# Kernel tuning notes

Hardware: AMD Instinct MI355X
Metric: run time of the kernel (lower is better)

Reference implementation:

```python
import jax, jax.numpy as jnp
from jax import lax
import numpy as np

B, H, W = 8, 256, 256
NH = 128          # num_hiddens
NRH = 32          # num_residual_hiddens
K = 1024          # num_embeddings
D = 128           # embedding_dim
CC = 0.25         # commitment_cost


def setup_inputs() -> dict:
    key = jax.random.key(0)
    ks = jax.random.split(key, 18)

    def w(k, shape):
        fan_in = int(np.prod(shape[1:]))
        return (jax.random.normal(k, shape, jnp.float32) / np.sqrt(fan_in)).astype(jnp.float32)

    inp = {
        "x": jax.random.normal(ks[0], (B, 3, H, W), jnp.float32),
        # encoder
        "enc_c1": w(ks[1], (NH // 2, 3, 4, 4)),        # conv4x4 s2
        "enc_c2": w(ks[2], (NH, NH // 2, 4, 4)),       # conv4x4 s2
        "enc_c3": w(ks[3], (NH, NH, 3, 3)),            # conv3x3
        "enc_r1a": w(ks[4], (NRH, NH, 3, 3)),
        "enc_r1b": w(ks[5], (NH, NRH, 1, 1)),
        "enc_r2a": w(ks[6], (NRH, NH, 3, 3)),
        "enc_r2b": w(ks[7], (NH, NRH, 1, 1)),
        "pre_vq_w": w(ks[8], (D, NH, 1, 1)),
        # codebook: uniform(-1/K, 1/K) as in original init
        "codebook": jax.random.uniform(ks[9], (K, D), jnp.float32, -1.0 / K, 1.0 / K),
        # decoder
        "dec_c1": w(ks[10], (NH, D, 3, 3)),
        "dec_r1a": w(ks[11], (NRH, NH, 3, 3)),
        "dec_r1b": w(ks[12], (NH, NRH, 1, 1)),
        "dec_r2a": w(ks[13], (NRH, NH, 3, 3)),
        "dec_r2b": w(ks[14], (NH, NRH, 1, 1)),
        # ConvTranspose2d weight, torch layout [Cin, Cout, 4, 4]
        "dec_dc": w(ks[15], (NH, NH // 2, 4, 4)),
        "dec_c3": w(ks[16], (3, NH // 2, 3, 3)),
    }
    return inp


def _conv(x, w, s, p):
    return lax.conv_general_dilated(x, w, (s, s), ((p, p), (p, p)),
                                    dimension_numbers=("NCHW", "OIHW", "NCHW"))


def _deconv4x4_s2_p1(x, w_t):
    # torch ConvTranspose2d(k=4, s=2, p=1): flip kernel, swap in/out, lhs-dilate
    w = jnp.transpose(w_t[:, :, ::-1, ::-1], (1, 0, 2, 3))  # [Cout, Cin, 4, 4]
    return lax.conv_general_dilated(x, w, (1, 1), ((2, 2), (2, 2)),
                                    lhs_dilation=(2, 2),
                                    dimension_numbers=("NCHW", "OIHW", "NCHW"))


def _res_stack(x, r1a, r1b, r2a, r2b):
    for a, b in ((r1a, r1b), (r2a, r2b)):
        h = _conv(jax.nn.relu(x), a, 1, 1)
        h = _conv(jax.nn.relu(h), b, 1, 0)
        x = x + h
    return jax.nn.relu(x)


def _resize1d_align(x, axis, out_size):
    n = x.shape[axis]
    pos = jnp.arange(out_size, dtype=jnp.float32) * ((n - 1) / (out_size - 1))
    lo = jnp.floor(pos).astype(jnp.int32)
    hi = jnp.minimum(lo + 1, n - 1)
    wt = (pos - lo.astype(jnp.float32)).astype(x.dtype)
    shape = [1] * x.ndim
    shape[axis] = out_size
    wt = wt.reshape(shape)
    return jnp.take(x, lo, axis=axis) * (1 - wt) + jnp.take(x, hi, axis=axis) * wt


def _upsample2x_bilinear_align(x):  # align_corners=True, separable
    x = _resize1d_align(x, 2, 2 * x.shape[2])
    return _resize1d_align(x, 3, 2 * x.shape[3])


def reference(x, enc_c1, enc_c2, enc_c3, enc_r1a, enc_r1b, enc_r2a, enc_r2b,
              pre_vq_w, codebook, dec_c1, dec_r1a, dec_r1b, dec_r2a, dec_r2b,
              dec_dc, dec_c3):
    # ---- encoder ----
    h = jax.nn.relu(_conv(x, enc_c1, 2, 1))
    h = jax.nn.relu(_conv(h, enc_c2, 2, 1))
    h = _conv(h, enc_c3, 1, 1)            # note: no relu here (matches source)
    h = _res_stack(h, enc_r1a, enc_r1b, enc_r2a, enc_r2b)
    z = _conv(h, pre_vq_w, 1, 0)          # [B, D, H/4, W/4]

    # ---- VQ (eval mode: no EMA update, q_latent_loss = 0) ----
    zp = jnp.transpose(z, (0, 2, 3, 1))               # [B, h, w, D]
    flat = zp.reshape(-1, D)                          # [N, D]
    dist = (jnp.sum(flat * flat, axis=1, keepdims=True)
            + jnp.sum(codebook * codebook, axis=1)
            - 2.0 * flat @ codebook.T)                # [N, K]
    idx = jnp.argmin(dist, axis=1)                    # [N]
    q = codebook[idx].reshape(zp.shape)               # gather lookup
    e_latent_loss = jnp.mean((lax.stop_gradient(q) - zp) ** 2)
    loss = CC * e_latent_loss
    q_st = zp + lax.stop_gradient(q - zp)             # straight-through
    counts = jnp.zeros((K,), jnp.float32).at[idx].add(1.0)
    avg_probs = counts / flat.shape[0]
    perplexity = jnp.exp(-jnp.sum(avg_probs * jnp.log(avg_probs + 1e-10)))
    quantized = jnp.transpose(q_st, (0, 3, 1, 2))     # [B, D, h, w]

    # ---- decoder ----
    d = _conv(quantized, dec_c1, 1, 1)
    d = _res_stack(d, dec_r1a, dec_r1b, dec_r2a, dec_r2b)
    d = jax.nn.relu(_deconv4x4_s2_p1(d, dec_dc))
    d = _upsample2x_bilinear_align(d)
    d = _conv(d, dec_c3, 1, 1)
    recon = 2.0 * jax.nn.sigmoid(d) - 1.0             # [B, 3, H, W]
    return loss, recon, perplexity
```

## Files before the change

kernel.cpp:

```cpp
#include <hip/hip_runtime.h>
#include <hip/hip_bf16.h>
#include <math.h>

#define CC_COST 0.25

typedef __attribute__((ext_vector_type(8))) short short8v;
typedef __attribute__((ext_vector_type(4))) float f32x4;
typedef __attribute__((ext_vector_type(16))) float f32x16;

__device__ __forceinline__ unsigned short f2bf(float f) {
    unsigned u = __float_as_uint(f);
    unsigned r = (u + 0x7FFFu + ((u >> 16) & 1u)) >> 16;
    return (unsigned short)r;
}
__device__ __forceinline__ float bf2f(unsigned short h) {
    return __uint_as_float(((unsigned)h) << 16);
}


struct WtJobs {
    const float* src[15];
    float* dst[15];
    int cout[15], cin[15], kk[15], kind[15];
    int blk0[16];
};

__global__ void wt_batch_k(WtJobs J)
{
    int blk = blockIdx.x;
    int j = 0;
    while (j < 14 && blk >= J.blk0[j + 1]) ++j;
    int i = (blk - J.blk0[j]) * 256 + threadIdx.x;
    int total = J.cout[j] * J.cin[j] * J.kk[j];
    if (i >= total) return;
    const float* src = J.src[j];
    float* dst = J.dst[j];
    int kind = J.kind[j];
    if (kind == 0) {
        int Cout = J.cout[j], Cin = J.cin[j], KK = J.kk[j];
        int oc = i % Cout; int t2 = i / Cout; int t = t2 % KK; int c = t2 / KK;
        dst[i] = src[(oc * Cin + c) * KK + t];
    } else {
        int o = i % 3; int t = (i / 3) % 9; int c = i / 27;
        dst[i] = src[(o * 64 + c) * 9 + t];
    }
}

__global__ void wt_split_k(const float* __restrict__ w,
                           unsigned short* __restrict__ whi,
                           unsigned short* __restrict__ wlo)
{
    int i = blockIdx.x * 256 + threadIdx.x;
    if (i >= 147456) return;
    int ci = i & 15;
    int oc = (i >> 4) & 127;
    int rest = i >> 11;
    int cb = rest & 7;
    int tap = rest >> 3;
    float v = w[(oc * 128 + cb * 16 + ci) * 9 + tap];
    unsigned short h = f2bf(v);
    whi[i] = h;
    wlo[i] = f2bf(v - bf2f(h));
}

__global__ void wt_split4_k(const float* __restrict__ w,
                            unsigned short* __restrict__ whi,
                            unsigned short* __restrict__ wlo)
{
    int i = blockIdx.x * 256 + threadIdx.x;
    if (i >= 131072) return;
    int t = i & 15;
    int oc = (i >> 4) & 127;
    int rest = i >> 11;
    int cb = rest & 3;
    int tap = rest >> 2;
    float v = w[(oc * 64 + cb * 16 + t) * 16 + tap];
    unsigned short h = f2bf(v);
    whi[i] = h;
    wlo[i] = f2bf(v - bf2f(h));
}

__global__ void wt_split_dc_k(const float* __restrict__ w,
                              unsigned short* __restrict__ whi,
                              unsigned short* __restrict__ wlo)
{
    int i = blockIdx.x * 256 + threadIdx.x;
    if (i >= 131072) return;
    int ci = i & 15;
    int oc = (i >> 4) & 63;
    int cb = (i >> 10) & 7;
    int kx = (i >> 13) & 3;
    int ky = i >> 15;
    float v = w[((size_t)(cb * 16 + ci) * 64 + oc) * 16 + ky * 4 + kx];
    unsigned short h = f2bf(v);
    whi[i] = h;
    wlo[i] = f2bf(v - bf2f(h));
}

__global__ void wt_split_r_k(const float* __restrict__ w,
                             unsigned short* __restrict__ whi,
                             unsigned short* __restrict__ wlo)
{
    int i = blockIdx.x * 256 + threadIdx.x;
    if (i >= 36864) return;
    int k5 = i & 31;
    int oc = (i >> 5) & 31;
    int cb = (i >> 10) & 3;
    int tap = i >> 12;
    float v = w[(oc * 128 + cb * 32 + k5) * 9 + tap];
    unsigned short h = f2bf(v);
    whi[i] = h;
    wlo[i] = f2bf(v - bf2f(h));
}

__global__ __launch_bounds__(512) void conv3x3_mfma(
    const float* __restrict__ in,
    const unsigned short* __restrict__ whi,
    const unsigned short* __restrict__ wlo,
    float* __restrict__ out)
{
    constexpr int CST = 40;
    __shared__ unsigned short ls_hi[4 * 68 * CST];
    __shared__ unsigned short ls_lo[4 * 68 * CST];

    int tid = threadIdx.x;
    int lane = tid & 63;
    int w = tid >> 6;
    int myrow = w & 1;
    int oc0 = (w >> 1) * 32;
    int y0 = (blockIdx.x & 31) * 2;
    int b  = blockIdx.x >> 5;
    int ln31 = lane & 31;
    int lhf  = lane >> 5;

    f32x16 acc0 = {};
    f32x16 acc1 = {};

    const float* inb = in + (size_t)b * 128 * 4096;

    for (int chunk = 0; chunk < 4; ++chunk) {
        int c0 = chunk * 32;
        __syncthreads();
        for (int i = tid; i < 4 * 66 * 16; i += 512) {
            int x = i % 66;
            int t = i / 66;
            int cp = t & 15;
            int r = t >> 4;
            int gy = y0 - 1 + r, gx = x - 1;
            float v0 = 0.f, v1 = 0.f;
            if ((unsigned)gy < 64u && (unsigned)gx < 64u) {
                const float* p = inb + (size_t)(c0 + 2 * cp) * 4096 + gy * 64 + gx;
                v0 = p[0];
                v1 = p[4096];
            }
            unsigned short h0 = f2bf(v0), h1 = f2bf(v1);
            unsigned short l0 = f2bf(v0 - bf2f(h0)), l1 = f2bf(v1 - bf2f(h1));
            int a = (r * 68 + x) * CST + 2 * cp;
            *reinterpret_cast<unsigned int*>(&ls_hi[a]) = (unsigned)h0 | ((unsigned)h1 << 16);
            *reinterpret_cast<unsigned int*>(&ls_lo[a]) = (unsigned)l0 | ((unsigned)l1 << 16);
        }
        __syncthreads();

        #pragma unroll
        for (int tap = 0; tap < 9; ++tap) {
            int dy = tap / 3, dx = tap - 3 * (tap / 3);
            int rbase = (myrow + dy) * 68;
            #pragma unroll
            for (int cb = 0; cb < 2; ++cb) {
                int cbg = chunk * 2 + cb;
                size_t wofs = (((size_t)tap * 8 + cbg) * 128 + oc0 + ln31) * 16 + lhf * 8;
                short8v ah = *reinterpret_cast<const short8v*>(whi + wofs);
                short8v al = *reinterpret_cast<const short8v*>(wlo + wofs);
                int k0 = cb * 16 + lhf * 8;
                int xo0 = (rbase + ln31 + dx) * CST + k0;
                int xo1 = (rbase + 32 + ln31 + dx) * CST + k0;
                short8v bh0 = *reinterpret_cast<const short8v*>(&ls_hi[xo0]);
                short8v bl0 = *reinterpret_cast<const short8v*>(&ls_lo[xo0]);
                short8v bh1 = *reinterpret_cast<const short8v*>(&ls_hi[xo1]);
                short8v bl1 = *reinterpret_cast<const short8v*>(&ls_lo[xo1]);
                acc0 = __builtin_amdgcn_mfma_f32_32x32x16_bf16(ah, bh0, acc0, 0, 0, 0);
                acc1 = __builtin_amdgcn_mfma_f32_32x32x16_bf16(ah, bh1, acc1, 0, 0, 0);
                acc0 = __builtin_amdgcn_mfma_f32_32x32x16_bf16(ah, bl0, acc0, 0, 0, 0);
                acc1 = __builtin_amdgcn_mfma_f32_32x32x16_bf16(ah, bl1, acc1, 0, 0, 0);
                acc0 = __builtin_amdgcn_mfma_f32_32x32x16_bf16(al, bh0, acc0, 0, 0, 0);
                acc1 = __builtin_amdgcn_mfma_f32_32x32x16_bf16(al, bh1, acc1, 0, 0, 0);
            }
        }
    }

    float* ob = out + (size_t)b * 128 * 4096 + (size_t)(y0 + myrow) * 64;
    #pragma unroll
    for (int r = 0; r < 16; ++r) {
        int oc = oc0 + (r & 3) + 8 * (r >> 2) + 4 * lhf;
        ob[(size_t)oc * 4096 + ln31]      = acc0[r];
        ob[(size_t)oc * 4096 + 32 + ln31] = acc1[r];
    }
}

__global__ __launch_bounds__(512) void conv4x4s2_mfma(
    const float* __restrict__ in,
    const unsigned short* __restrict__ whi,
    const unsigned short* __restrict__ wlo,
    float* __restrict__ out)
{
    constexpr int CST = 24;
    __shared__ unsigned short lsEh[6 * 65 * CST];
    __shared__ unsigned short lsEl[6 * 65 * CST];
    __shared__ unsigned short lsOh[6 * 65 * CST];
    __shared__ unsigned short lsOl[6 * 65 * CST];

    int tid = threadIdx.x;
    int lane = tid & 63;
    int w = tid >> 6;
    int myrow = w & 1;
    int oc0 = (w >> 1) * 32;
    int y0 = (blockIdx.x & 31) * 2;
    int b  = blockIdx.x >> 5;
    int ln31 = lane & 31;
    int lhf  = lane >> 5;

    f32x16 acc0 = {};
    f32x16 acc1 = {};

    const float* inb = in + (size_t)b * 64 * 16384;

    for (int cb = 0; cb < 4; ++cb) {
        int c0 = cb * 16;
        __syncthreads();
        for (int i = tid; i < 12480; i += 512) {
            int gxi = i % 130; int t2 = i / 130;
            int r = t2 % 6; int cc = t2 / 6;
            int gx = gxi - 1;
            int gy = 2 * y0 - 1 + r;
            float v = 0.f;
            if ((unsigned)gy < 128u && (unsigned)gx < 128u)
                v = inb[(size_t)(c0 + cc) * 16384 + gy * 128 + gx];
            unsigned short h = f2bf(v);
            unsigned short l = f2bf(v - bf2f(h));
            if (gx & 1) {
                int a = (r * 65 + ((gx + 1) >> 1)) * CST + cc;
                lsOh[a] = h; lsOl[a] = l;
            } else {
                int a = (r * 65 + (gx >> 1)) * CST + cc;
                lsEh[a] = h; lsEl[a] = l;
            }
        }
        __syncthreads();

        #pragma unroll
        for (int tap = 0; tap < 16; ++tap) {
            int ky = tap >> 2, kx = tap & 3;
            int ridx = 2 * myrow + ky;
            int dlt = kx >> 1;
            const unsigned short* ph = (kx & 1) ? lsEh : lsOh;
            const unsigned short* pl = (kx & 1) ? lsEl : lsOl;
            size_t aoff = ((size_t)((tap * 4 + cb) * 128 + oc0 + ln31)) * 16 + lhf * 8;
            short8v ah = *reinterpret_cast<const short8v*>(whi + aoff);
            short8v al = *reinterpret_cast<const short8v*>(wlo + aoff);
            int base0 = (ridx * 65 + ln31 + dlt) * CST + lhf * 8;
            int base1 = (ridx * 65 + 32 + ln31 + dlt) * CST + lhf * 8;
            short8v bh0 = *reinterpret_cast<const short8v*>(ph + base0);
            short8v bl0 = *reinterpret_cast<const short8v*>(pl + base0);
            short8v bh1 = *reinterpret_cast<const short8v*>(ph + base1);
            short8v bl1 = *reinterpret_cast<const short8v*>(pl + base1);
            acc0 = __builtin_amdgcn_mfma_f32_32x32x16_bf16(ah, bh0, acc0, 0, 0, 0);
            acc1 = __builtin_amdgcn_mfma_f32_32x32x16_bf16(ah, bh1, acc1, 0, 0, 0);
            acc0 = __builtin_amdgcn_mfma_f32_32x32x16_bf16(ah, bl0, acc0, 0, 0, 0);
            acc1 = __builtin_amdgcn_mfma_f32_32x32x16_bf16(ah, bl1, acc1, 0, 0, 0);
            acc0 = __builtin_amdgcn_mfma_f32_32x32x16_bf16(al, bh0, acc0, 0, 0, 0);
            acc1 = __builtin_amdgcn_mfma_f32_32x32x16_bf16(al, bh1, acc1, 0, 0, 0);
        }
    }

    int y = y0 + myrow;
    float* ob = out + (size_t)b * 128 * 4096 + (size_t)y * 64;
    #pragma unroll
    for (int r = 0; r < 16; ++r) {
        int oc = oc0 + (r & 3) + 8 * (r >> 2) + 4 * lhf;
        ob[(size_t)oc * 4096 + ln31]      = fmaxf(acc0[r], 0.f);
        ob[(size_t)oc * 4096 + 32 + ln31] = fmaxf(acc1[r], 0.f);
    }
}

__global__ __launch_bounds__(512) void deconv_mfma(
    const float* __restrict__ in,
    const unsigned short* __restrict__ whi,
    const unsigned short* __restrict__ wlo,
    float* __restrict__ out)
{
    constexpr int CST = 40;
    __shared__ unsigned short ls_hi[3 * 68 * CST];
    __shared__ unsigned short ls_lo[3 * 68 * CST];

    int tid = threadIdx.x;
    int lane = tid & 63;
    int w = tid >> 6;
    int myrow = w & 1;
    int oc0 = ((w >> 1) & 1) * 32;
    int oxp = w >> 2;
    int yb = blockIdx.x & 63;
    int b  = blockIdx.x >> 6;
    int ln31 = lane & 31;
    int lhf  = lane >> 5;

    f32x16 acc0 = {};
    f32x16 acc1 = {};

    const float* inb = in + (size_t)b * 128 * 4096;

    for (int chunk = 0; chunk < 4; ++chunk) {
        int c0 = chunk * 32;
        __syncthreads();
        for (int i = tid; i < 3 * 66 * 16; i += 512) {
            int x = i % 66;
            int t = i / 66;
            int cp = t & 15;
            int r = t >> 4;
            int gy = yb - 1 + r, gx = x - 1;
            float v0 = 0.f, v1 = 0.f;
            if ((unsigned)gy < 64u && (unsigned)gx < 64u) {
                const float* p = inb + (size_t)(c0 + 2 * cp) * 4096 + gy * 64 + gx;
                v0 = fmaxf(p[0], 0.f);
                v1 = fmaxf(p[4096], 0.f);
            }
            unsigned short h0 = f2bf(v0), h1 = f2bf(v1);
            unsigned short l0 = f2bf(v0 - bf2f(h0)), l1 = f2bf(v1 - bf2f(h1));
            int a = (r * 68 + x) * CST + 2 * cp;
            *reinterpret_cast<unsigned int*>(&ls_hi[a]) = (unsigned)h0 | ((unsigned)h1 << 16);
            *reinterpret_cast<unsigned int*>(&ls_lo[a]) = (unsigned)l0 | ((unsigned)l1 << 16);
        }
        __syncthreads();

        #pragma unroll
        for (int tki = 0; tki < 2; ++tki) {
            int ky = (1 - myrow) + 2 * tki;
            int ldsrow = 1 + myrow - tki;
            #pragma unroll
            for (int txi = 0; txi < 2; ++txi) {
                int kx = (1 - oxp) + 2 * txi;
                int dlt = oxp - txi;
                #pragma unroll
                for (int cb = 0; cb < 2; ++cb) {
                    int cbg = chunk * 2 + cb;
                    size_t aoff = ((size_t)(((ky * 4 + kx) * 8 + cbg) * 64 + oc0 + ln31)) * 16 + lhf * 8;
                    short8v ah = *reinterpret_cast<const short8v*>(whi + aoff);
                    short8v al = *reinterpret_cast<const short8v*>(wlo + aoff);
                    int k0 = cb * 16 + lhf * 8;
                    int xo0 = (ldsrow * 68 + ln31 + dlt + 1) * CST + k0;
                    int xo1 = (ldsrow * 68 + 32 + ln31 + dlt + 1) * CST + k0;
                    short8v bh0 = *reinterpret_cast<const short8v*>(&ls_hi[xo0]);
                    short8v bl0 = *reinterpret_cast<const short8v*>(&ls_lo[xo0]);
                    short8v bh1 = *reinterpret_cast<const short8v*>(&ls_hi[xo1]);
                    short8v bl1 = *reinterpret_cast<const short8v*>(&ls_lo[xo1]);
                    acc0 = __builtin_amdgcn_mfma_f32_32x32x16_bf16(ah, bh0, acc0, 0, 0, 0);
                    acc1 = __builtin_amdgcn_mfma_f32_32x32x16_bf16(ah, bh1, acc1, 0, 0, 0);
                    acc0 = __builtin_amdgcn_mfma_f32_32x32x16_bf16(ah, bl0, acc0, 0, 0, 0);
                    acc1 = __builtin_amdgcn_mfma_f32_32x32x16_bf16(ah, bl1, acc1, 0, 0, 0);
                    acc0 = __builtin_amdgcn_mfma_f32_32x32x16_bf16(al, bh0, acc0, 0, 0, 0);
                    acc1 = __builtin_amdgcn_mfma_f32_32x32x16_bf16(al, bh1, acc1, 0, 0, 0);
                }
            }
        }
    }

    int oy = 2 * yb + myrow;
    float* ob = out + (size_t)b * 64 * 16384 + (size_t)oy * 128;
    #pragma unroll
    for (int r = 0; r < 16; ++r) {
        int oc = oc0 + (r & 3) + 8 * (r >> 2) + 4 * lhf;
        ob[(size_t)oc * 16384 + oxp + 2 * ln31]      = fmaxf(acc0[r], 0.f);
        ob[(size_t)oc * 16384 + oxp + 64 + 2 * ln31] = fmaxf(acc1[r], 0.f);
    }
}

__global__ __launch_bounds__(512) void conv3x3r_mfma(
    const float* __restrict__ in,
    const unsigned short* __restrict__ whi,
    const unsigned short* __restrict__ wlo,
    float* __restrict__ out)
{
    constexpr int CST = 40;
    __shared__ unsigned short ls_hi[3 * 68 * CST];
    __shared__ unsigned short ls_lo[3 * 68 * CST];

    int tid = threadIdx.x;
    int lane = tid & 63;
    int w = tid >> 6;
    int oc0 = (w & 1) * 16;
    int px0 = (w >> 1) * 16;
    int y = blockIdx.x & 63;
    int b = blockIdx.x >> 6;
    int n16 = lane & 15;
    int kk4 = lane >> 4;

    f32x4 acc = {};

    const float* inb = in + (size_t)b * 128 * 4096;

    for (int cb = 0; cb < 4; ++cb) {
        int c0 = cb * 32;
        __syncthreads();
        for (int i = tid; i < 3 * 66 * 16; i += 512) {
            int x = i % 66;
            int t = i / 66;
            int cp = t & 15;
            int r = t >> 4;
            int gy = y - 1 + r, gx = x - 1;
            float v0 = 0.f, v1 = 0.f;
            if ((unsigned)gy < 64u && (unsigned)gx < 64u) {
                const float* p = inb + (size_t)(c0 + 2 * cp) * 4096 + gy * 64 + gx;
                v0 = fmaxf(p[0], 0.f);
                v1 = fmaxf(p[4096], 0.f);
            }
            unsigned short h0 = f2bf(v0), h1 = f2bf(v1);
            unsigned short l0 = f2bf(v0 - bf2f(h0)), l1 = f2bf(v1 - bf2f(h1));
            int a = (r * 68 + x) * CST + 2 * cp;
            *reinterpret_cast<unsigned int*>(&ls_hi[a]) = (unsigned)h0 | ((unsigned)h1 << 16);
            *reinterpret_cast<unsigned int*>(&ls_lo[a]) = (unsigned)l0 | ((unsigned)l1 << 16);
        }
        __syncthreads();

        #pragma unroll
        for (int tap = 0; tap < 9; ++tap) {
            int dy = tap / 3, dx = tap - 3 * (tap / 3);
            size_t aoff = ((size_t)((tap * 4 + cb) * 32 + oc0 + n16)) * 32 + kk4 * 8;
            short8v ah = *reinterpret_cast<const short8v*>(whi + aoff);
            short8v al = *reinterpret_cast<const short8v*>(wlo + aoff);
            int xo = (dy * 68 + px0 + n16 + dx) * CST + kk4 * 8;
            short8v bh = *reinterpret_cast<const short8v*>(&ls_hi[xo]);
            short8v bl = *reinterpret_cast<const short8v*>(&ls_lo[xo]);
            acc = __builtin_amdgcn_mfma_f32_16x16x32_bf16(ah, bh, acc, 0, 0, 0);
            acc = __builtin_amdgcn_mfma_f32_16x16x32_bf16(ah, bl, acc, 0, 0, 0);
            acc = __builtin_amdgcn_mfma_f32_16x16x32_bf16(al, bh, acc, 0, 0, 0);
        }
    }

    float* ob = out + (size_t)b * 32 * 4096 + (size_t)y * 64;
    #pragma unroll
    for (int r = 0; r < 4; ++r) {
        int oc = oc0 + kk4 * 4 + r;
        ob[(size_t)oc * 4096 + px0 + n16] = acc[r];
    }
}

template<int CIN, int COUT, int CC, bool IN_RELU, bool ADD_RES>
__global__ __launch_bounds__(256) void conv1x1_k(
    const float* __restrict__ in, const float* __restrict__ wT,
    const float* __restrict__ res, float* __restrict__ out)
{
    static_assert(COUT == 128, "tile assumes 128");
    __shared__ __align__(16) float ls_in[CC][64];
    __shared__ __align__(16) float ls_w[CC][COUT];
    int tid = threadIdx.x;
    int pxg = tid & 7, ocg = tid >> 3;
    int x0 = pxg * 8, oc0 = ocg * 4;
    int y = blockIdx.x & 63, b = blockIdx.x >> 6;

    float acc[4][8];
    #pragma unroll
    for (int o = 0; o < 4; ++o)
        #pragma unroll
        for (int p = 0; p < 8; ++p) acc[o][p] = 0.f;

    for (int c0 = 0; c0 < CIN; c0 += CC) {
        __syncthreads();
        for (int i = tid; i < CC * 64; i += 256) {
            int xx = i & 63, cc = i >> 6;
            float v = in[(((size_t)b * CIN + c0 + cc) * 64 + y) * 64 + xx];
            if (IN_RELU) v = fmaxf(v, 0.f);
            ls_in[cc][xx] = v;
        }
        const float* wsrc = wT + (size_t)c0 * COUT;
        for (int i = tid; i < CC * COUT; i += 256)
            (&ls_w[0][0])[i] = wsrc[i];
        __syncthreads();

        for (int cc = 0; cc < CC; ++cc) {
            float rv[8];
            const float* base = &ls_in[cc][x0];
            float4 v0 = *reinterpret_cast<const float4*>(base);
            float4 v1 = *reinterpret_cast<const float4*>(base + 4);
            rv[0]=v0.x; rv[1]=v0.y; rv[2]=v0.z; rv[3]=v0.w;
            rv[4]=v1.x; rv[5]=v1.y; rv[6]=v1.z; rv[7]=v1.w;
            float4 w4 = *reinterpret_cast<const float4*>(&ls_w[cc][oc0]);
            float wv[4] = {w4.x, w4.y, w4.z, w4.w};
            #pragma unroll
            for (int p = 0; p < 8; ++p)
                #pragma unroll
                for (int o = 0; o < 4; ++o)
                    acc[o][p] = fmaf(rv[p], wv[o], acc[o][p]);
        }
    }
    #pragma unroll
    for (int o = 0; o < 4; ++o) {
        float* op = out + (((size_t)b * COUT + oc0 + o) * 64 + y) * 64 + x0;
        const float* rp = res + (((size_t)b * COUT + oc0 + o) * 64 + y) * 64 + x0;
        #pragma unroll
        for (int q = 0; q < 2; ++q) {
            float4 v = make_float4(acc[o][4*q], acc[o][4*q+1],
                                   acc[o][4*q+2], acc[o][4*q+3]);
            if (ADD_RES) {
                float4 r4 = *reinterpret_cast<const float4*>(rp + 4 * q);
                v.x += r4.x; v.y += r4.y; v.z += r4.z; v.w += r4.w;
            }
            *reinterpret_cast<float4*>(op + 4 * q) = v;
        }
    }
}

template<int CIN, int COUT, int WOUT, int CC, int OCB, int WOC, int NSLICE>
__global__ __launch_bounds__(256) void conv4x4s2_k(
    const float* __restrict__ in, const float* __restrict__ wT,
    float* __restrict__ out)
{
    constexpr int WIN = WOUT * 2;
    constexpr int NPXG = WOUT / 8, NOCG = COUT / OCB;
    static_assert(NPXG * NOCG == 256, "bad tile");
    constexpr int WUSE = 2 * WOUT + 2;
    constexpr int PADLEN = ((WUSE + (WUSE / 16 + 1) * 4) + 3) & ~3;
    __shared__ __align__(16) float ls_in[CC][4][PADLEN];
    __shared__ __align__(16) float ls_w[CC][16][COUT];

    int tid = threadIdx.x;
    int pxg = tid % NPXG, ocg = tid / NPXG;
    int x0 = pxg * 8, oc0 = ocg * OCB;
    int blk = blockIdx.x;
    int y = blk % WOUT; int rest = blk / WOUT;
    int slice = rest % NSLICE; int b = rest / NSLICE;
    int oc_base = slice * COUT;
    const float* inb = in + (size_t)b * CIN * WIN * WIN;

    float acc[OCB][8];
    #pragma unroll
    for (int o = 0; o < OCB; ++o)
        #pragma unroll
        for (int p = 0; p < 8; ++p) acc[o][p] = 0.f;

    for (int c0 = 0; c0 < CIN; c0 += CC) {
        __syncthreads();
        for (int i = tid; i < CC * 4 * WUSE; i += 256) {
            int xx = i % WUSE; int t = i / WUSE; int r = t & 3; int cc = t >> 2;
            int gy = 2 * y - 1 + r, gx = xx - 1;
            float v = 0.f;
            if ((unsigned)gy < (unsigned)WIN && (unsigned)gx < (unsigned)WIN)
                v = inb[(c0 + cc) * WIN * WIN + gy * WIN + gx];
            ls_in[cc][r][xx + ((xx >> 4) << 2)] = v;
        }
        const float* wsrc = wT + (size_t)c0 * 16 * WOC + oc_base;
        for (int i = tid; i < CC * 16 * COUT; i += 256) {
            int o = i % COUT; int tt = (i / COUT) % 16; int cc = i / (16 * COUT);
            ls_w[cc][tt][o] = wsrc[(cc * 16 + tt) * WOC + o];
        }
        __syncthreads();

        for (int cc = 0; cc < CC; ++cc) {
            const float* lw = &ls_w[cc][0][0];
            #pragma unroll
            for (int ky = 0; ky < 4; ++ky) {
                float rv[18];
                const float* base = &ls_in[cc][ky][20 * pxg];
                #pragma unroll
                for (int q = 0; q < 4; ++q) {
                    float4 v = *reinterpret_cast<const float4*>(base + 4 * q);
                    rv[4*q]=v.x; rv[4*q+1]=v.y; rv[4*q+2]=v.z; rv[4*q+3]=v.w;
                }
                rv[16] = base[20]; rv[17] = base[21];
                #pragma unroll
                for (int kx = 0; kx < 4; ++kx) {
                    const float* wp = lw + (ky * 4 + kx) * COUT + oc0;
                    float wv[OCB];
                    if constexpr (OCB == 4) {
                        float4 w4 = *reinterpret_cast<const float4*>(wp);
                        wv[0]=w4.x; wv[1]=w4.y; wv[2]=w4.z; wv[3]=w4.w;
                    } else {
                        float2 w2 = *reinterpret_cast<const float2*>(wp);
                        wv[0]=w2.x; wv[1]=w2.y;
                    }
                    #pragma unroll
                    for (int p = 0; p < 8; ++p) {
                        float iv = rv[2 * p + kx];
                        #pragma unroll
                        for (int o = 0; o < OCB; ++o)
                            acc[o][p] = fmaf(iv, wv[o], acc[o][p]);
                    }
                }
            }
        }
    }
    #pragma unroll
    for (int o = 0; o < OCB; ++o) {
        float* op = out + (((size_t)b * (COUT * NSLICE) + oc_base + oc0 + o) * WOUT + y) * WOUT + x0;
        #pragma unroll
        for (int q = 0; q < 2; ++q) {
            float4 v = make_float4(fmaxf(acc[o][4*q],0.f), fmaxf(acc[o][4*q+1],0.f),
                                   fmaxf(acc[o][4*q+2],0.f), fmaxf(acc[o][4*q+3],0.f));
            *reinterpret_cast<float4*>(op + 4 * q) = v;
        }
    }
}

template<int CC>
__global__ __launch_bounds__(256) void upconv_k(
    const float* __restrict__ in,
    const float* __restrict__ wT3,
    float* __restrict__ out)
{
    __shared__ __align__(16) float ls_u[CC][6][132];
    __shared__ float ls_w[64 * 27];
    __shared__ float xfx[132];
    __shared__ int   xloT[132];

    int tid = threadIdx.x;
    int row = tid >> 6;
    int pxl = tid & 63;
    int blk = blockIdx.x;
    int xh = blk & 1;
    int yblk = (blk >> 1) & 63;
    int b = blk >> 7;
    int xbase = xh * 128;
    int y0 = yblk * 4, y = y0 + row;
    const float SCL = 127.0f / 255.0f;
    const float* hb = in + (size_t)b * 64 * 16384;

    for (int i = tid; i < 1728; i += 256) ls_w[i] = wT3[i];
    if (tid < 130) {
        int ux = xbase - 1 + tid;
        bool v = ((unsigned)ux < 256u);
        float px = (v ? ux : 0) * SCL;
        int lo = (int)px;
        xloT[tid] = lo;
        xfx[tid] = v ? (px - (float)lo) : -1.0f;
    }

    float acc[3][2];
    #pragma unroll
    for (int o = 0; o < 3; ++o) { acc[o][0] = 0.f; acc[o][1] = 0.f; }

    for (int c0 = 0; c0 < 64; c0 += CC) {
        __syncthreads();
        for (int i = tid; i < CC * 6 * 130; i += 256) {
            int xx = i % 130; int t = i / 130; int r = t % 6; int cc = t / 6;
            int uy = y0 - 1 + r;
            float v = 0.f;
            float fx = xfx[xx];
            if ((unsigned)uy < 256u && fx >= 0.f) {
                float py = uy * SCL;
                int ylo = (int)py; int yhi = min(ylo + 1, 127); float fy = py - (float)ylo;
                int lo = xloT[xx]; int hi = min(lo + 1, 127);
                const float* hp = hb + (size_t)(c0 + cc) * 16384 + ylo * 128;
                const float* hq = hb + (size_t)(c0 + cc) * 16384 + yhi * 128;
                float a = hp[lo], b2 = hp[hi], c2 = hq[lo], d2 = hq[hi];
                float top = a + (b2 - a) * fx;
                float bot = c2 + (d2 - c2) * fx;
                v = top + (bot - top) * fy;
            }
            ls_u[cc][r][xx] = v;
        }
        __syncthreads();

        for (int cc = 0; cc < CC; ++cc) {
            #pragma unroll
            for (int j = 0; j < 3; ++j) {
                const float* base = &ls_u[cc][row + j][pxl * 2];
                float2 a0 = *reinterpret_cast<const float2*>(base);
                float2 a1 = *reinterpret_cast<const float2*>(base + 2);
                float rv[4] = {a0.x, a0.y, a1.x, a1.y};
                #pragma unroll
                for (int i2 = 0; i2 < 3; ++i2) {
                    const float* wp = &ls_w[((c0 + cc) * 9 + (j * 3 + i2)) * 3];
                    float w0 = wp[0], w1 = wp[1], w2 = wp[2];
                    #pragma unroll
                    for (int p = 0; p < 2; ++p) {
                        float iv = rv[p + i2];
                        acc[0][p] = fmaf(iv, w0, acc[0][p]);
                        acc[1][p] = fmaf(iv, w1, acc[1][p]);
                        acc[2][p] = fmaf(iv, w2, acc[2][p]);
                    }
                }
            }
        }
    }
    int x0 = xbase + pxl * 2;
    #pragma unroll
    for (int o = 0; o < 3; ++o) {
        float2 v;
        v.x = 2.f / (1.f + expf(-acc[o][0])) - 1.f;
        v.y = 2.f / (1.f + expf(-acc[o][1])) - 1.f;
        float* op = out + (((size_t)b * 3 + o) * 256 + y) * 256 + x0;
        *reinterpret_cast<float2*>(op) = v;
    }
}

__global__ void prep_codebook(const float* __restrict__ cb,
                              unsigned short* __restrict__ cbh,
                              unsigned short* __restrict__ cbl,
                              float* __restrict__ ce2,
                              unsigned int* __restrict__ counts)
{
    int k = blockIdx.x * 256 + threadIdx.x;
    if (k >= 1024) return;
    float s = 0.f;
    for (int d = 0; d < 128; ++d) {
        float v = cb[k * 128 + d];
        s = fmaf(v, v, s);
        unsigned short h = f2bf(v);
        int kk = d >> 4, t = d & 15;
        cbh[(kk * 1024 + k) * 16 + t] = h;
        cbl[(kk * 1024 + k) * 16 + t] = f2bf(v - bf2f(h));
    }
    ce2[k] = s;
    counts[k] = 0u;
}

__global__ __launch_bounds__(512) void vq_fused(
    const float* __restrict__ z, const float* __restrict__ cb,
    const unsigned short* __restrict__ cbh,
    const unsigned short* __restrict__ cbl,
    const float* __restrict__ ce2,
    unsigned int* __restrict__ counts, float* __restrict__ q,
    double* __restrict__ partial)
{
    constexpr int ZP = 136;
    __shared__ unsigned short zh[64 * ZP];
    __shared__ unsigned short zlo[64 * ZP];
    __shared__ float ce2l[1024];
    __shared__ float cmbd[4][2][32];
    __shared__ int   cmbi[4][2][32];
    __shared__ int sidx[64];
    __shared__ float red[8];

    int tid = threadIdx.x;
    int lane = tid & 63;
    int w = tid >> 6;
    int pxg = w & 1;
    int cgrp = w >> 1;
    int ln31 = lane & 31;
    int lhf = lane >> 5;
    int p0g = blockIdx.x * 64;
    int b = p0g >> 12;
    int p0 = p0g & 4095;

    for (int i = tid; i < 8192; i += 512) {
        int d = i >> 6, px = i & 63;
        float v = z[((size_t)b * 128 + d) * 4096 + p0 + px];
        unsigned short h = f2bf(v);
        zh[px * ZP + d]  = h;
        zlo[px * ZP + d] = f2bf(v - bf2f(h));
    }
    for (int i = tid; i < 1024; i += 512) ce2l[i] = ce2[i];
    __syncthreads();

    int pxrow = pxg * 32 + ln31;
    short8v zfh[8], zfl[8];
    #pragma unroll
    for (int kk = 0; kk < 8; ++kk) {
        int off = pxrow * ZP + kk * 16 + lhf * 8;
        zfh[kk] = *reinterpret_cast<const short8v*>(&zh[off]);
        zfl[kk] = *reinterpret_cast<const short8v*>(&zlo[off]);
    }

    float best = 3.4e38f; int bidx = 0;
    #pragma unroll
    for (int ct = 0; ct < 8; ++ct) {
        int c0 = cgrp * 256 + ct * 32;
        f32x16 acc = {};
        #pragma unroll
        for (int kk = 0; kk < 8; ++kk) {
            size_t aoff = ((size_t)(kk * 1024 + c0 + ln31)) * 16 + lhf * 8;
            short8v ah = *reinterpret_cast<const short8v*>(cbh + aoff);
            short8v al = *reinterpret_cast<const short8v*>(cbl + aoff);
            acc = __builtin_amdgcn_mfma_f32_32x32x16_bf16(ah, zfh[kk], acc, 0, 0, 0);
            acc = __builtin_amdgcn_mfma_f32_32x32x16_bf16(ah, zfl[kk], acc, 0, 0, 0);
            acc = __builtin_amdgcn_mfma_f32_32x32x16_bf16(al, zfh[kk], acc, 0, 0, 0);
        }
        #pragma unroll
        for (int r = 0; r < 16; ++r) {
            int code = c0 + (r & 3) + 8 * (r >> 2) + 4 * lhf;
            float dist = ce2l[code] - 2.f * acc[r];
            if (dist < best || (dist == best && code < bidx)) { best = dist; bidx = code; }
        }
    }
    {
        float ob = __shfl_xor(best, 32);
        int   oi = __shfl_xor(bidx, 32);
        if (ob < best || (ob == best && oi < bidx)) { best = ob; bidx = oi; }
    }
    if (lane < 32) { cmbd[cgrp][pxg][lane] = best; cmbi[cgrp][pxg][lane] = bidx; }
    __syncthreads();
    if (tid < 64) {
        int pg = tid >> 5, l = tid & 31;
        float bv = cmbd[0][pg][l]; int bi = cmbi[0][pg][l];
        #pragma unroll
        for (int g = 1; g < 4; ++g) {
            float ov = cmbd[g][pg][l]; int oi = cmbi[g][pg][l];
            if (ov < bv || (ov == bv && oi < bi)) { bv = ov; bi = oi; }
        }
        sidx[pg * 32 + l] = bi;
        atomicAdd(&counts[bi], 1u);
    }
    __syncthreads();

    int pix = tid & 63, dg = tid >> 6;
    int kidx = sidx[pix];
    const float* crow = cb + (size_t)kidx * 128 + dg * 16;
    float sq = 0.f;
    size_t zbase = ((size_t)b * 128 + dg * 16) * 4096 + p0 + pix;
    #pragma unroll
    for (int ii = 0; ii < 4; ++ii) {
        float4 c4 = *reinterpret_cast<const float4*>(crow + 4 * ii);
        float vals[4] = {c4.x, c4.y, c4.z, c4.w};
        #pragma unroll
        for (int jj = 0; jj < 4; ++jj) {
            int dl = ii * 4 + jj;
            float qv = vals[jj];
            float zv = z[zbase + (size_t)dl * 4096];
            float df = qv - zv;
            sq = fmaf(df, df, sq);
            q[zbase + (size_t)dl * 4096] = qv;
        }
    }
    #pragma unroll
    for (int off = 32; off > 0; off >>= 1) sq += __shfl_xor(sq, off);
    if (lane == 0) red[w] = sq;
    __syncthreads();
    if (tid == 0) {
        double s = 0.0;
        #pragma unroll
        for (int ww = 0; ww < 8; ++ww) s += (double)red[ww];
        partial[blockIdx.x] = s;
    }
}

__global__ __launch_bounds__(256) void finalize_kernel(
    const double* __restrict__ partial, const unsigned int* __restrict__ counts,
    float* __restrict__ dout)
{
    __shared__ double sd[256];
    __shared__ double lossSh;
    int tid = threadIdx.x;
    double s = 0.0;
    for (int i = tid; i < 512; i += 256) s += partial[i];
    sd[tid] = s; __syncthreads();
    for (int off = 128; off > 0; off >>= 1) {
        if (tid < off) sd[tid] += sd[tid + off];
        __syncthreads();
    }
    if (tid == 0) lossSh = CC_COST * sd[0] / 4194304.0;
    __syncthreads();

    double h = 0.0;
    for (int k = tid; k < 1024; k += 256) {
        double pp = (double)counts[k] / 32768.0;
        h += pp * log(pp + 1e-10);
    }
    sd[tid] = h; __syncthreads();
    for (int off = 128; off > 0; off >>= 1) {
        if (tid < off) sd[tid] += sd[tid + off];
        __syncthreads();
    }
    if (tid == 0) {
        dout[0]       = (float)lossSh;
        dout[1572865] = (float)exp(-sd[0]);
    }
}

extern "C" void kernel_launch(void* const* d_in, const int* in_sizes, int n_in,
                              void* d_out, int out_size, void* d_ws, size_t ws_size,
                              hipStream_t stream)
{
    const float* x        = (const float*)d_in[0];
    const float* enc_c1   = (const float*)d_in[1];
    const float* enc_c2   = (const float*)d_in[2];
    const float* enc_c3   = (const float*)d_in[3];
    const float* enc_r1a  = (const float*)d_in[4];
    const float* enc_r1b  = (const float*)d_in[5];
    const float* enc_r2a  = (const float*)d_in[6];
    const float* enc_r2b  = (const float*)d_in[7];
    const float* pre_vq_w = (const float*)d_in[8];
    const float* codebook = (const float*)d_in[9];
    const float* dec_c1   = (const float*)d_in[10];
    const float* dec_r1a  = (const float*)d_in[11];
    const float* dec_r1b  = (const float*)d_in[12];
    const float* dec_r2a  = (const float*)d_in[13];
    const float* dec_r2b  = (const float*)d_in[14];
    const float* dec_dc   = (const float*)d_in[15];
    const float* dec_c3   = (const float*)d_in[16];
    float* dout = (float*)d_out;

    char* wsp = (char*)d_ws;
    auto alloc = [&](size_t bytes) {
        void* p = (void*)wsp;
        wsp += (bytes + 255) & ~(size_t)255;
        return p;
    };
    float* h1   = (float*)alloc(8ull*64*128*128*4);
    float* bufA = (float*)alloc(8ull*128*64*64*4);
    float* bufB = (float*)alloc(8ull*128*64*64*4);
    float* bufT = (float*)alloc(8ull*32*64*64*4);
    unsigned short* cbh = (unsigned short*)alloc(131072*2);
    unsigned short* cbl = (unsigned short*)alloc(131072*2);
    float* ce2  = (float*)alloc(1024*4);
    unsigned int* counts = (unsigned int*)alloc(1024*4);
    double* partial = (double*)alloc(512*8);
    float* wt_ec1  = (float*)alloc(3072*4);
    float* wt_er1b = (float*)alloc(4096*4);
    float* wt_er2b = (float*)alloc(4096*4);
    float* wt_pvq  = (float*)alloc(16384*4);
    float* wt_dr1b = (float*)alloc(4096*4);
    float* wt_dr2b = (float*)alloc(4096*4);
    float* wt_dc3  = (float*)alloc(1728*4);
    unsigned short* w3hi_e = (unsigned short*)alloc(147456*2);
    unsigned short* w3lo_e = (unsigned short*)alloc(147456*2);
    unsigned short* w3hi_d = (unsigned short*)alloc(147456*2);
    unsigned short* w3lo_d = (unsigned short*)alloc(147456*2);
    unsigned short* w4hi   = (unsigned short*)alloc(131072*2);
    unsigned short* w4lo   = (unsigned short*)alloc(131072*2);
    unsigned short* wdchi  = (unsigned short*)alloc(131072*2);
    unsigned short* wdclo  = (unsigned short*)alloc(131072*2);
    unsigned short* wr1aeh = (unsigned short*)alloc(36864*2);
    unsigned short* wr1ael = (unsigned short*)alloc(36864*2);
    unsigned short* wr2aeh = (unsigned short*)alloc(36864*2);
    unsigned short* wr2ael = (unsigned short*)alloc(36864*2);
    unsigned short* wr1adh = (unsigned short*)alloc(36864*2);
    unsigned short* wr1adl = (unsigned short*)alloc(36864*2);
    unsigned short* wr2adh = (unsigned short*)alloc(36864*2);
    unsigned short* wr2adl = (unsigned short*)alloc(36864*2);
    float* zb = bufA;
    float* qb = h1;

    prep_codebook<<<4, 256, 0, stream>>>(codebook, cbh, cbl, ce2, counts);

    WtJobs J;
    const float* srcs[7] = {enc_c1, enc_r1b, enc_r2b, pre_vq_w,
                            dec_r1b, dec_r2b, dec_c3};
    float* dsts[7] = {wt_ec1, wt_er1b, wt_er2b, wt_pvq,
                      wt_dr1b, wt_dr2b, wt_dc3};
    int couts[7] = {64, 128, 128, 128, 128, 128, 3};
    int cins[7]  = {3, 32, 32, 128, 32, 32, 64};
    int kks[7]   = {16, 1, 1, 1, 1, 1, 9};
    int kinds[7] = {0, 0, 0, 0, 0, 0, 2};
    int off = 0;
    for (int j = 0; j < 7; ++j) {
        J.src[j] = srcs[j]; J.dst[j] = dsts[j];
        J.cout[j] = couts[j]; J.cin[j] = cins[j]; J.kk[j] = kks[j];
        J.kind[j] = kinds[j];
        J.blk0[j] = off;
        off += (couts[j] * cins[j] * kks[j] + 255) / 256;
    }
    J.blk0[7] = off;
    for (int j = 8; j < 16; ++j) J.blk0[j] = off + 1000000;
    wt_batch_k<<<off, 256, 0, stream>>>(J);
    wt_split_k<<<576, 256, 0, stream>>>(enc_c3, w3hi_e, w3lo_e);
    wt_split_k<<<576, 256, 0, stream>>>(dec_c1, w3hi_d, w3lo_d);
    wt_split4_k<<<512, 256, 0, stream>>>(enc_c2, w4hi, w4lo);
    wt_split_dc_k<<<512, 256, 0, stream>>>(dec_dc, wdchi, wdclo);
    wt_split_r_k<<<144, 256, 0, stream>>>(enc_r1a, wr1aeh, wr1ael);
    wt_split_r_k<<<144, 256, 0, stream>>>(enc_r2a, wr2aeh, wr2ael);
    wt_split_r_k<<<144, 256, 0, stream>>>(dec_r1a, wr1adh, wr1adl);
    wt_split_r_k<<<144, 256, 0, stream>>>(dec_r2a, wr2adh, wr2adl);

    conv4x4s2_k<3, 64, 128, 3, 4, 64, 1><<<1024, 256, 0, stream>>>(x, wt_ec1, h1);
    conv4x4s2_mfma<<<256, 512, 0, stream>>>(h1, w4hi, w4lo, bufA);
    conv3x3_mfma<<<256, 512, 0, stream>>>(bufA, w3hi_e, w3lo_e, bufB);
    conv3x3r_mfma<<<512, 512, 0, stream>>>(bufB, wr1aeh, wr1ael, bufT);
    conv1x1_k<32, 128, 32, true, true><<<512, 256, 0, stream>>>(bufT, wt_er1b, bufB, bufB);
    conv3x3r_mfma<<<512, 512, 0, stream>>>(bufB, wr2aeh, wr2ael, bufT);
    conv1x1_k<32, 128, 32, true, true><<<512, 256, 0, stream>>>(bufT, wt_er2b, bufB, bufB);
    conv1x1_k<128, 128, 32, true, false><<<512, 256, 0, stream>>>(bufB, wt_pvq, bufB, zb);

    vq_fused<<<512, 512, 0, stream>>>(zb, codebook, cbh, cbl, ce2, counts, qb, partial);

    conv3x3_mfma<<<256, 512, 0, stream>>>(qb, w3hi_d, w3lo_d, bufA);
    conv3x3r_mfma<<<512, 512, 0, stream>>>(bufA, wr1adh, wr1adl, bufT);
    conv1x1_k<32, 128, 32, true, true><<<512, 256, 0, stream>>>(bufT, wt_dr1b, bufA, bufA);
    conv3x3r_mfma<<<512, 512, 0, stream>>>(bufA, wr2adh, wr2adl, bufT);
    conv1x1_k<32, 128, 32, true, true><<<512, 256, 0, stream>>>(bufT, wt_dr2b, bufA, bufA);
    deconv_mfma<<<512, 512, 0, stream>>>(bufA, wdchi, wdclo, h1);
    upconv_k<8><<<1024, 256, 0, stream>>>(h1, wt_dc3, dout + 1);

    finalize_kernel<<<1, 256, 0, stream>>>(partial, counts, dout);
}
```

Baseline: 788.3 us.

## Fuse residual 3x3 and 1x1 convs into one MFMA kernel; retile upconv

Each residual block's 3x3 conv (128->32) and 1x1 conv (32->128) plus residual add now run in one kernel. The intermediate goes through LDS as split bf16 hi/lo and feeds a 32x32 MFMA with precomputed split 1x1 weights. This removes the bufT round trip and four kernel launches, and the result is written to a ping-pong buffer instead of in place. Separately, upconv now computes one pixel per thread over 2 rows with a smaller channel chunk and twice the blocks. That trades some register reuse for lower LDS use and more parallelism.

```diff
diff --git a/kernel.cpp b/kernel.cpp
--- a/kernel.cpp
+++ b/kernel.cpp
@@ -108,6 +108,21 @@
     int cb = (i >> 10) & 3;
     int tap = i >> 12;
     float v = w[(oc * 128 + cb * 32 + k5) * 9 + tap];
+    unsigned short h = f2bf(v);
+    whi[i] = h;
+    wlo[i] = f2bf(v - bf2f(h));
+}
+
+__global__ void wt_split_1x1_k(const float* __restrict__ w,
+                               unsigned short* __restrict__ whi,
+                               unsigned short* __restrict__ wlo)
+{
+    int i = blockIdx.x * 256 + threadIdx.x;
+    if (i >= 4096) return;
+    int ci = i & 15;
+    int oc = (i >> 4) & 127;
+    int kk = i >> 11;
+    float v = w[oc * 32 + kk * 16 + ci];
     unsigned short h = f2bf(v);
     whi[i] = h;
     wlo[i] = f2bf(v - bf2f(h));
@@ -373,10 +388,12 @@
     }
 }
 
-__global__ __launch_bounds__(512) void conv3x3r_mfma(
+__global__ __launch_bounds__(512) void fused_res_k(
     const float* __restrict__ in,
     const unsigned short* __restrict__ whi,
     const unsigned short* __restrict__ wlo,
+    const unsigned short* __restrict__ w1hi,
+    const unsigned short* __restrict__ w1lo,
     float* __restrict__ out)
 {
     constexpr int CST = 40;
@@ -392,9 +409,10 @@
     int b = blockIdx.x >> 6;
     int n16 = lane & 15;
     int kk4 = lane >> 4;
+    int ln31 = lane & 31;
+    int lhf = lane >> 5;
 
     f32x4 acc = {};
-
     const float* inb = in + (size_t)b * 128 * 4096;
 
     for (int cb = 0; cb < 4; ++cb) {
@@ -435,11 +453,41 @@
         }
     }
 
-    float* ob = out + (size_t)b * 32 * 4096 + (size_t)y * 64;
+    __syncthreads();
     #pragma unroll
     for (int r = 0; r < 4; ++r) {
-        int oc = oc0 + kk4 * 4 + r;
-        ob[(size_t)oc * 4096 + px0 + n16] = acc[r];
+        int ch = oc0 + kk4 * 4 + r;
+        int px = px0 + n16;
+        float v = fmaxf(acc[r], 0.f);
+        unsigned short h = f2bf(v);
+        ls_hi[px * CST + ch] = h;
+        ls_lo[px * CST + ch] = f2bf(v - bf2f(h));
+    }
+    __syncthreads();
+
+    int oc1 = (w & 3) * 32;
+    int pxt = (w >> 2) * 32;
+    f32x16 acc2 = {};
+    #pragma unroll
+    for (int kk = 0; kk < 2; ++kk) {
+        size_t aoff = ((size_t)(kk * 128 + oc1 + ln31)) * 16 + lhf * 8;
+        short8v ah = *reinterpret_cast<const short8v*>(w1hi + aoff);
+        short8v al = *reinterpret_cast<const short8v*>(w1lo + aoff);
+        int boff = (pxt + ln31) * CST + kk * 16 + lhf * 8;
+        short8v bh = *reinterpret_cast<const short8v*>(&ls_hi[boff]);
+        short8v bl = *reinterpret_cast<const short8v*>(&ls_lo[boff]);
+        acc2 = __builtin_amdgcn_mfma_f32_32x32x16_bf16(ah, bh, acc2, 0, 0, 0);
+        acc2 = __builtin_amdgcn_mfma_f32_32x32x16_bf16(ah, bl, acc2, 0, 0, 0);
+        acc2 = __builtin_amdgcn_mfma_f32_32x32x16_bf16(al, bh, acc2, 0, 0, 0);
+    }
+
+    float* ob = out + (size_t)b * 128 * 4096 + (size_t)y * 64;
+    const float* rb = inb + (size_t)y * 64;
+    #pragma unroll
+    for (int r = 0; r < 16; ++r) {
+        int oc = oc1 + (r & 3) + 8 * (r >> 2) + 4 * lhf;
+        size_t o = (size_t)oc * 4096 + pxt + ln31;
+        ob[o] = rb[o] + acc2[r];
     }
 }
 
@@ -605,20 +653,20 @@
     const float* __restrict__ wT3,
     float* __restrict__ out)
 {
-    __shared__ __align__(16) float ls_u[CC][6][132];
+    __shared__ __align__(16) float ls_u[CC][4][132];
     __shared__ float ls_w[64 * 27];
     __shared__ float xfx[132];
     __shared__ int   xloT[132];
 
     int tid = threadIdx.x;
-    int row = tid >> 6;
-    int pxl = tid & 63;
+    int row = tid >> 7;
+    int pxl = tid & 127;
     int blk = blockIdx.x;
     int xh = blk & 1;
-    int yblk = (blk >> 1) & 63;
-    int b = blk >> 7;
+    int yblk = (blk >> 1) & 127;
+    int b = blk >> 8;
     int xbase = xh * 128;
-    int y0 = yblk * 4, y = y0 + row;
+    int y0 = yblk * 2, y = y0 + row;
     const float SCL = 127.0f / 255.0f;
     const float* hb = in + (size_t)b * 64 * 16384;
 
@@ -632,14 +680,12 @@
         xfx[tid] = v ? (px - (float)lo) : -1.0f;
     }
 
-    float acc[3][2];
-    #pragma unroll
-    for (int o = 0; o < 3; ++o) { acc[o][0] = 0.f; acc[o][1] = 0.f; }
+    float acc[3] = {0.f, 0.f, 0.f};
 
     for (int c0 = 0; c0 < 64; c0 += CC) {
         __syncthreads();
-        for (int i = tid; i < CC * 6 * 130; i += 256) {
-            int xx = i % 130; int t = i / 130; int r = t % 6; int cc = t / 6;
+        for (int i = tid; i < CC * 4 * 130; i += 256) {
+            int xx = i % 130; int t = i / 130; int r = t & 3; int cc = t >> 2;
             int uy = y0 - 1 + r;
             float v = 0.f;
             float fx = xfx[xx];
@@ -661,33 +707,26 @@
         for (int cc = 0; cc < CC; ++cc) {
             #pragma unroll
             for (int j = 0; j < 3; ++j) {
-                const float* base = &ls_u[cc][row + j][pxl * 2];
-                float2 a0 = *reinterpret_cast<const float2*>(base);
-                float2 a1 = *reinterpret_cast<const float2*>(base + 2);
-                float rv[4] = {a0.x, a0.y, a1.x, a1.y};
-                #pragma unroll
-                for (int i2 = 0; i2 < 3; ++i2) {
-                    const float* wp = &ls_w[((c0 + cc) * 9 + (j * 3 + i2)) * 3];
-                    float w0 = wp[0], w1 = wp[1], w2 = wp[2];
-                    #pragma unroll
-                    for (int p = 0; p < 2; ++p) {
-                        float iv = rv[p + i2];
-                        acc[0][p] = fmaf(iv, w0, acc[0][p]);
-                        acc[1][p] = fmaf(iv, w1, acc[1][p]);
-                        acc[2][p] = fmaf(iv, w2, acc[2][p]);
-                    }
-                }
+                const float* urow = &ls_u[cc][row + j][pxl];
+                float r0 = urow[0], r1 = urow[1], r2 = urow[2];
+                const float* wb = &ls_w[((c0 + cc) * 9 + j * 3) * 3];
+                acc[0] = fmaf(r0, wb[0], acc[0]);
+                acc[1] = fmaf(r0, wb[1], acc[1]);
+                acc[2] = fmaf(r0, wb[2], acc[2]);
+                acc[0] = fmaf(r1, wb[3], acc[0]);
+                acc[1] = fmaf(r1, wb[4], acc[1]);
+                acc[2] = fmaf(r1, wb[5], acc[2]);
+                acc[0] = fmaf(r2, wb[6], acc[0]);
+                acc[1] = fmaf(r2, wb[7], acc[1]);
+                acc[2] = fmaf(r2, wb[8], acc[2]);
             }
         }
     }
-    int x0 = xbase + pxl * 2;
+    int x0 = xbase + pxl;
     #pragma unroll
     for (int o = 0; o < 3; ++o) {
-        float2 v;
-        v.x = 2.f / (1.f + expf(-acc[o][0])) - 1.f;
-        v.y = 2.f / (1.f + expf(-acc[o][1])) - 1.f;
-        float* op = out + (((size_t)b * 3 + o) * 256 + y) * 256 + x0;
-        *reinterpret_cast<float2*>(op) = v;
+        float v = 2.f / (1.f + expf(-acc[o])) - 1.f;
+        out[(((size_t)b * 3 + o) * 256 + y) * 256 + x0] = v;
     }
 }
 
@@ -896,18 +935,13 @@
     float* h1   = (float*)alloc(8ull*64*128*128*4);
     float* bufA = (float*)alloc(8ull*128*64*64*4);
     float* bufB = (float*)alloc(8ull*128*64*64*4);
-    float* bufT = (float*)alloc(8ull*32*64*64*4);
     unsigned short* cbh = (unsigned short*)alloc(131072*2);
     unsigned short* cbl = (unsigned short*)alloc(131072*2);
     float* ce2  = (float*)alloc(1024*4);
     unsigned int* counts = (unsigned int*)alloc(1024*4);
     double* partial = (double*)alloc(512*8);
     float* wt_ec1  = (float*)alloc(3072*4);
-    float* wt_er1b = (float*)alloc(4096*4);
-    float* wt_er2b = (float*)alloc(4096*4);
     float* wt_pvq  = (float*)alloc(16384*4);
-    float* wt_dr1b = (float*)alloc(4096*4);
-    float* wt_dr2b = (float*)alloc(4096*4);
     float* wt_dc3  = (float*)alloc(1728*4);
     unsigned short* w3hi_e = (unsigned short*)alloc(147456*2);
     unsigned short* w3lo_e = (unsigned short*)alloc(147456*2);
@@ -925,30 +959,36 @@
     unsigned short* wr1adl = (unsigned short*)alloc(36864*2);
     unsigned short* wr2adh = (unsigned short*)alloc(36864*2);
     unsigned short* wr2adl = (unsigned short*)alloc(36864*2);
+    unsigned short* w1e1h  = (unsigned short*)alloc(4096*2);
+    unsigned short* w1e1l  = (unsigned short*)alloc(4096*2);
+    unsigned short* w1e2h  = (unsigned short*)alloc(4096*2);
+    unsigned short* w1e2l  = (unsigned short*)alloc(4096*2);
+    unsigned short* w1d1h  = (unsigned short*)alloc(4096*2);
+    unsigned short* w1d1l  = (unsigned short*)alloc(4096*2);
+    unsigned short* w1d2h  = (unsigned short*)alloc(4096*2);
+    unsigned short* w1d2l  = (unsigned short*)alloc(4096*2);
     float* zb = bufA;
     float* qb = h1;
 
     prep_codebook<<<4, 256, 0, stream>>>(codebook, cbh, cbl, ce2, counts);
 
     WtJobs J;
-    const float* srcs[7] = {enc_c1, enc_r1b, enc_r2b, pre_vq_w,
-                            dec_r1b, dec_r2b, dec_c3};
-    float* dsts[7] = {wt_ec1, wt_er1b, wt_er2b, wt_pvq,
-                      wt_dr1b, wt_dr2b, wt_dc3};
-    int couts[7] = {64, 128, 128, 128, 128, 128, 3};
-    int cins[7]  = {3, 32, 32, 128, 32, 32, 64};
-    int kks[7]   = {16, 1, 1, 1, 1, 1, 9};
-    int kinds[7] = {0, 0, 0, 0, 0, 0, 2};
+    const float* srcs[3] = {enc_c1, pre_vq_w, dec_c3};
+    float* dsts[3] = {wt_ec1, wt_pvq, wt_dc3};
+    int couts[3] = {64, 128, 3};
+    int cins[3]  = {3, 128, 64};
+    int kks[3]   = {16, 1, 9};
+    int kinds[3] = {0, 0, 2};
     int off = 0;
-    for (int j = 0; j < 7; ++j) {
+    for (int j = 0; j < 3; ++j) {
         J.src[j] = srcs[j]; J.dst[j] = dsts[j];
         J.cout[j] = couts[j]; J.cin[j] = cins[j]; J.kk[j] = kks[j];
         J.kind[j] = kinds[j];
         J.blk0[j] = off;
         off += (couts[j] * cins[j] * kks[j] + 255) / 256;
     }
-    J.blk0[7] = off;
-    for (int j = 8; j < 16; ++j) J.blk0[j] = off + 1000000;
+    J.blk0[3] = off;
+    for (int j = 4; j < 16; ++j) J.blk0[j] = off + 1000000;
     wt_batch_k<<<off, 256, 0, stream>>>(J);
     wt_split_k<<<576, 256, 0, stream>>>(enc_c3, w3hi_e, w3lo_e);
     wt_split_k<<<576, 256, 0, stream>>>(dec_c1, w3hi_d, w3lo_d);
@@ -958,25 +998,25 @@
     wt_split_r_k<<<144, 256, 0, stream>>>(enc_r2a, wr2aeh, wr2ael);
     wt_split_r_k<<<144, 256, 0, stream>>>(dec_r1a, wr1adh, wr1adl);
     wt_split_r_k<<<144, 256, 0, stream>>>(dec_r2a, wr2adh, wr2adl);
+    wt_split_1x1_k<<<16, 256, 0, stream>>>(enc_r1b, w1e1h, w1e1l);
+    wt_split_1x1_k<<<16, 256, 0, stream>>>(enc_r2b, w1e2h, w1e2l);
+    wt_split_1x1_k<<<16, 256, 0, stream>>>(dec_r1b, w1d1h, w1d1l);
+    wt_split_1x1_k<<<16, 256, 0, stream>>>(dec_r2b, w1d2h, w1d2l);
 
     conv4x4s2_k<3, 64, 128, 3, 4, 64, 1><<<1024, 256, 0, stream>>>(x, wt_ec1, h1);
     conv4x4s2_mfma<<<256, 512, 0, stream>>>(h1, w4hi, w4lo, bufA);
     conv3x3_mfma<<<256, 512, 0, stream>>>(bufA, w3hi_e, w3lo_e, bufB);
-    conv3x3r_mfma<<<512, 512, 0, stream>>>(bufB, wr1aeh, wr1ael, bufT);
-    conv1x1_k<32, 128, 32, true, true><<<512, 256, 0, stream>>>(bufT, wt_er1b, bufB, bufB);
-    conv3x3r_mfma<<<512, 512, 0, stream>>>(bufB, wr2aeh, wr2ael, bufT);
-    conv1x1_k<32, 128, 32, true, true><<<512, 256, 0, stream>>>(bufT, wt_er2b, bufB, bufB);
+    fused_res_k<<<512, 512, 0, stream>>>(bufB, wr1aeh, wr1ael, w1e1h, w1e1l, bufA);
+    fused_res_k<<<512, 512, 0, stream>>>(bufA, wr2aeh, wr2ael, w1e2h, w1e2l, bufB);
     conv1x1_k<128, 128, 32, true, false><<<512, 256, 0, stream>>>(bufB, wt_pvq, bufB, zb);
 
     vq_fused<<<512, 512, 0, stream>>>(zb, codebook, cbh, cbl, ce2, counts, qb, partial);
 
     conv3x3_mfma<<<256, 512, 0, stream>>>(qb, w3hi_d, w3lo_d, bufA);
-    conv3x3r_mfma<<<512, 512, 0, stream>>>(bufA, wr1adh, wr1adl, bufT);
-    conv1x1_k<32, 128, 32, true, true><<<512, 256, 0, stream>>>(bufT, wt_dr1b, bufA, bufA);
-    conv3x3r_mfma<<<512, 512, 0, stream>>>(bufA, wr2adh, wr2adl, bufT);
-    conv1x1_k<32, 128, 32, true, true><<<512, 256, 0, stream>>>(bufT, wt_dr2b, bufA, bufA);
+    fused_res_k<<<512, 512, 0, stream>>>(bufA, wr1adh, wr1adl, w1d1h, w1d1l, bufB);
+    fused_res_k<<<512, 512, 0, stream>>>(bufB, wr2adh, wr2adl, w1d2h, w1d2l, bufA);
     deconv_mfma<<<512, 512, 0, stream>>>(bufA, wdchi, wdclo, h1);
-    upconv_k<8><<<1024, 256, 0, stream>>>(h1, wt_dc3, dout + 1);
+    upconv_k<4><<<2048, 256, 0, stream>>>(h1, wt_dc3, dout + 1);
 
     finalize_kernel<<<1, 256, 0, stream>>>(partial, counts, dout);
 }
```

New measurement: 759.5 us. 1.04x faster.
